# Kernel tuning notes

Hardware: AMD Instinct MI355X
Metric: run time of the kernel (lower is better)

## Reference

```python
import jax, jax.numpy as jnp
import numpy as np

N_NODES = 50000
N_GRAPHS = 100
NPG = 500          # nodes per graph
PAIRS = 2000       # undirected (src>dst) pairs per graph
E = N_GRAPHS * PAIRS * 2  # each pair duplicated with class 0/1 -> 400000 edges


def setup_inputs() -> dict:
    rng = np.random.default_rng(0)
    a = rng.integers(0, NPG, size=(N_GRAPHS, PAIRS))
    b = rng.integers(0, NPG - 1, size=(N_GRAPHS, PAIRS))
    b = b + (b >= a)                               # ensure b != a
    hi = np.maximum(a, b); lo = np.minimum(a, b)   # hi > lo  (src > dst)
    off = (np.arange(N_GRAPHS) * NPG)[:, None]
    hi = (hi + off).ravel(); lo = (lo + off).ravel()
    order = np.lexsort((lo, hi))                   # pre-sort by (row, col) -> sort_edge_index is identity
    hi, lo = hi[order], lo[order]
    src = np.repeat(hi, 2); dst = np.repeat(lo, 2)
    edges = np.stack([src, dst]).astype(np.int32)  # [2, E]
    weights = rng.random(E).astype(np.float32)
    classes = np.tile(np.array([0.0, 1.0], np.float32), E // 2)
    edge_attr = np.stack([weights, classes], axis=1)  # [E, 2]
    batch_labels = np.repeat(np.arange(N_GRAPHS), NPG).astype(np.int32)
    detector_labels = np.ones(N_NODES, dtype=bool)

    key = jax.random.key(0)
    ks = jax.random.split(key, 16)
    def lin(k, i, o):
        return jax.random.normal(k, (i, o), jnp.float32) * 0.1
    dims = [5, 32, 64, 128]
    p = {}
    for l in range(3):
        p[f"Wrel{l}"] = lin(ks[3 * l], dims[l], dims[l + 1])
        p[f"brel{l}"] = jnp.zeros((dims[l + 1],), jnp.float32)
        p[f"Wroot{l}"] = lin(ks[3 * l + 1], dims[l], dims[l + 1])
    p["Wd0"] = lin(ks[9], 257, 128); p["bd0"] = jnp.zeros((128,), jnp.float32)
    p["gnw0"] = jnp.ones((128,), jnp.float32); p["gnb0"] = jnp.zeros((128,), jnp.float32); p["gnms0"] = jnp.ones((128,), jnp.float32)
    p["Wd1"] = lin(ks[10], 128, 64); p["bd1"] = jnp.zeros((64,), jnp.float32)
    p["gnw1"] = jnp.ones((64,), jnp.float32); p["gnb1"] = jnp.zeros((64,), jnp.float32); p["gnms1"] = jnp.ones((64,), jnp.float32)
    p["Wout"] = lin(ks[11], 64, 1); p["bout"] = jnp.zeros((1,), jnp.float32)

    x = jax.random.normal(ks[12], (N_NODES, 5), jnp.float32)
    return dict(x=x, edges=jnp.asarray(edges), edge_attr=jnp.asarray(edge_attr),
                detector_labels=jnp.asarray(detector_labels),
                batch_labels=jnp.asarray(batch_labels), n_graphs=N_GRAPHS, **p)


def reference(x, edges, edge_attr, detector_labels, batch_labels, n_graphs,
              Wrel0, brel0, Wroot0, Wrel1, brel1, Wroot1, Wrel2, brel2, Wroot2,
              Wd0, bd0, gnw0, gnb0, gnms0, Wd1, bd1, gnw1, gnb1, gnms1, Wout, bout):
    N = x.shape[0]
    src, dst = edges[0], edges[1]
    w = edge_attr[:, :1]  # [E,1] edge weight

    # --- PyG GraphConv stack: out = segsum_dst(w * x[src]) @ W_rel + b_rel + x @ W_root ---
    for Wr, br, Wrt in ((Wrel0, brel0, Wroot0), (Wrel1, brel1, Wroot1), (Wrel2, brel2, Wroot2)):
        msg = x[src] * w                                   # gather + scale
        agg = jax.ops.segment_sum(msg, dst, num_segments=N)
        x = jnp.tanh(agg @ Wr + br + x @ Wrt)

    # --- SplitSyndromes: all nodes are detectors and all edges have src>dst by
    # construction, so the boolean compaction is the identity; sort_edge_index
    # is a stable sort by (row, col) ---
    order = jnp.lexsort((dst, src))
    src, dst = src[order], dst[order]
    ea = edge_attr[order]
    w = ea[:, :1]
    # (class_embd / weight_embd branches in the original are dead code: `c` is never used)

    feat = jnp.concatenate([x[src], w, x[dst]], axis=-1)   # [E, 257]
    eb = batch_labels[src]                                  # per-edge graph id

    def gnorm(h, wgt, bias, ms):
        # PyG GraphNorm: (h - mean*mean_scale) / sqrt(E[(h-mean*ms)^2] + 1e-5) * w + b, per graph
        cnt = jax.ops.segment_sum(jnp.ones(h.shape[0], h.dtype), eb, num_segments=n_graphs)
        mean = jax.ops.segment_sum(h, eb, num_segments=n_graphs) / cnt[:, None]
        out = h - mean[eb] * ms
        var = jax.ops.segment_sum(out * out, eb, num_segments=n_graphs) / cnt[:, None]
        return wgt * out / jnp.sqrt(var + 1e-5)[eb] + bias

    feat = gnorm(jnp.tanh(feat @ Wd0 + bd0), gnw0, gnb0, gnms0)
    feat = gnorm(jnp.tanh(feat @ Wd1 + bd1), gnw1, gnb1, gnms1)
    feat = feat @ Wout + bout                               # [E, 1]

    # --- pair consecutive (class 0/1) duplicates, take min, segment softmax ---
    pair = jnp.concatenate([feat[::2], feat[1::2]], axis=1)           # [E/2, 2]
    classes = jnp.stack([ea[::2, 1], ea[1::2, 1]], axis=1)           # [E/2, 2]
    vals = jnp.min(pair, axis=1)
    inds = jnp.argmin(pair, axis=1)
    edge_classes = jnp.take_along_axis(classes, inds[:, None], axis=1)[:, 0]
    out_edges = jnp.stack([src[::2], dst[::2]])
    ebp = batch_labels[src[::2]]
    m = jax.ops.segment_max(vals, ebp, num_segments=n_graphs)
    z = jnp.exp(vals - m[ebp])
    denom = jax.ops.segment_sum(z, ebp, num_segments=n_graphs)
    p = z / (denom[ebp] + 1e-16)                            # PyG softmax eps
    return out_edges, p, edge_classes
```

## Files before the change

### kernel.cpp

```cpp
#include <hip/hip_runtime.h>


#define N_NODES 50000
#define N_EDGES 400000
#define N_PAIRS 200000
#define N_G     100
#define EPG     4000
#define PPG     2000
#define NCHUNK  3125

typedef float  f4   __attribute__((ext_vector_type(4)));
typedef short  bf8  __attribute__((ext_vector_type(8)));
typedef unsigned u32x4 __attribute__((ext_vector_type(4)));
typedef unsigned short ushort_t;

__device__ __forceinline__ float tanh_fast(float x) {
    float cx = fminf(15.f, fmaxf(-15.f, x));
    float e = __expf(2.f * cx);
    return (e - 1.f) * __builtin_amdgcn_rcpf(e + 1.f);
}
__device__ __forceinline__ unsigned f2bf(float f) {
    unsigned u = __float_as_uint(f);
    return (u + 0x7FFFu + ((u >> 16) & 1u)) >> 16;
}
__device__ __forceinline__ float bf2f(unsigned h) { return __uint_as_float(h << 16); }

__global__ void k_csr_count(const int* __restrict__ edges, int* __restrict__ cnt) {
    int p = blockIdx.x * 256 + threadIdx.x;
    if (p >= N_PAIRS) return;
    atomicAdd(&cnt[edges[N_EDGES + 2 * p]], 1);
}
__global__ __launch_bounds__(512) void k_csr_scan(const int* __restrict__ cnt,
                                                  int* __restrict__ offs) {
    __shared__ int s[512];
    int g = blockIdx.x, t = threadIdx.x;
    int v = (t < 500) ? cnt[g * 500 + t] : 0;
    s[t] = v; __syncthreads();
    for (int off = 1; off < 512; off <<= 1) {
        int a = (t >= off) ? s[t - off] : 0;
        __syncthreads();
        s[t] += a; __syncthreads();
    }
    if (t < 500) offs[g * 500 + t] = g * PPG + s[t] - v;
}
__global__ void k_csr_fill(const int* __restrict__ edges, const float* __restrict__ ea,
                           const int* __restrict__ offs, int* __restrict__ fillc,
                           int* __restrict__ esrc, float* __restrict__ ew) {
    int p = blockIdx.x * 256 + threadIdx.x;
    if (p >= N_PAIRS) return;
    int d = edges[N_EDGES + 2 * p];
    int pos = offs[d] + atomicAdd(&fillc[d], 1);
    esrc[pos] = edges[2 * p];
    ew[pos] = ea[4 * p] + ea[4 * p + 2];
}

__global__ __launch_bounds__(256) void k_gath5(
    const int* __restrict__ cnt, const int* __restrict__ offs,
    const int* __restrict__ esrc, const float* __restrict__ ew,
    const float* __restrict__ x, float* __restrict__ agg) {
    int t = blockIdx.x * 256 + threadIdx.x;
    int n = t >> 3, k = t & 7;
    if (n >= N_NODES || k >= 5) return;
    int o0 = offs[n], c = cnt[n];
    float acc = 0.f;
    for (int i = o0; i < o0 + c; ++i) acc += x[esrc[i] * 5 + k] * ew[i];
    agg[n * 5 + k] = acc;
}
__global__ __launch_bounds__(256) void k_gath32(
    const int* __restrict__ cnt, const int* __restrict__ offs,
    const int* __restrict__ esrc, const float* __restrict__ ew,
    const float* __restrict__ x1, ushort_t* __restrict__ c2h, ushort_t* __restrict__ c2l) {
    int n = blockIdx.x * 8 + (threadIdx.x >> 5), k = threadIdx.x & 31;
    if (n >= N_NODES) return;
    int o0 = offs[n], c = cnt[n];
    float acc = 0.f;
    for (int i = o0; i < o0 + c; ++i) acc += x1[esrc[i] * 32 + k] * ew[i];
    unsigned hi = f2bf(acc);
    size_t o = (size_t)n * 64 + k;
    c2h[o] = (ushort_t)hi;
    c2l[o] = (ushort_t)f2bf(acc - bf2f(hi));
}
__global__ __launch_bounds__(256) void k_gath64(
    const int* __restrict__ cnt, const int* __restrict__ offs,
    const int* __restrict__ esrc, const float* __restrict__ ew,
    const float* __restrict__ x2, ushort_t* __restrict__ ch, ushort_t* __restrict__ cl) {
    int n = blockIdx.x * 4 + (threadIdx.x >> 6), k = threadIdx.x & 63;
    if (n >= N_NODES) return;
    int o0 = offs[n], c = cnt[n];
    float acc = 0.f;
    for (int i = o0; i < o0 + c; ++i) acc += x2[esrc[i] * 64 + k] * ew[i];
    unsigned hi = f2bf(acc);
    size_t o = (size_t)n * 128 + k;
    ch[o] = (ushort_t)hi;
    cl[o] = (ushort_t)f2bf(acc - bf2f(hi));
}

__global__ __launch_bounds__(256) void k_dense1(
    const float* __restrict__ x, const float* __restrict__ agg,
    const float* __restrict__ Wrel, const float* __restrict__ brel,
    const float* __restrict__ Wroot, float* __restrict__ x1,
    ushort_t* __restrict__ c2h, ushort_t* __restrict__ c2l) {
    __shared__ float wr[160], wt[160], bb[32];
    __shared__ float sa[8][5], sx[8][5];
    for (int i = threadIdx.x; i < 160; i += 256) { wr[i] = Wrel[i]; wt[i] = Wroot[i]; }
    if (threadIdx.x < 32) bb[threadIdx.x] = brel[threadIdx.x];
    int j = threadIdx.x & 31, nl = threadIdx.x >> 5;
    int nb = blockIdx.x * 8;
    __syncthreads();
    for (int i = threadIdx.x; i < 40; i += 256) {
        int nn = nb + i / 5, kk = i % 5;
        float av = 0.f, xv = 0.f;
        if (nn < N_NODES) { av = agg[nn * 5 + kk]; xv = x[nn * 5 + kk]; }
        sa[i / 5][kk] = av; sx[i / 5][kk] = xv;
    }
    __syncthreads();
    int n = nb + nl;
    if (n < N_NODES) {
        float acc = bb[j];
        #pragma unroll
        for (int k = 0; k < 5; ++k)
            acc += sa[nl][k] * wr[k * 32 + j] + sx[nl][k] * wt[k * 32 + j];
        float v = tanhf(acc);
        x1[n * 32 + j] = v;
        unsigned hi = f2bf(v);
        size_t o = (size_t)n * 64 + 32 + j;
        c2h[o] = (ushort_t)hi;
        c2l[o] = (ushort_t)f2bf(v - bf2f(hi));
    }
}

__global__ void k_packWc(const float* __restrict__ Wrel2, const float* __restrict__ Wroot2,
                         unsigned* __restrict__ dst) {
    int i = blockIdx.x * 256 + threadIdx.x;
    int t = i & 3, l = (i >> 2) & 63, kk = (i >> 8) & 3, n = i >> 10;
    int k = kk * 32 + ((l >> 4) << 3) + 2 * t;
    int j = 16 * n + (l & 15);
    float v0 = (k < 64) ? Wrel2[k * 128 + j] : Wroot2[(k - 64) * 128 + j];
    float v1 = (k + 1 < 64) ? Wrel2[(k + 1) * 128 + j] : Wroot2[(k + 1 - 64) * 128 + j];
    dst[i] = f2bf(v0) | (f2bf(v1) << 16);
}
__global__ void k_packWpq(const float* __restrict__ Wd0, unsigned* __restrict__ dst) {
    int i = blockIdx.x * 256 + threadIdx.x;
    int t = i & 3, l = (i >> 2) & 63, kk = (i >> 8) & 3, n = i >> 10;
    int k = kk * 32 + ((l >> 4) << 3) + 2 * t;
    int j = 16 * n + (l & 15);
    float v0 = (j < 128) ? Wd0[k * 128 + j] : Wd0[(129 + k) * 128 + (j - 128)];
    float v1 = (j < 128) ? Wd0[(k + 1) * 128 + j] : Wd0[(129 + k + 1) * 128 + (j - 128)];
    dst[i] = f2bf(v0) | (f2bf(v1) << 16);
}
__global__ void k_packW2(const float* __restrict__ Wrel1, const float* __restrict__ Wroot1,
                         unsigned* __restrict__ dst) {
    int i = blockIdx.x * 256 + threadIdx.x;
    int t = i & 3, l = (i >> 2) & 63, kk = (i >> 8) & 1, n = i >> 9;
    int k = kk * 32 + ((l >> 4) << 3) + 2 * t;
    int j = 16 * n + (l & 15);
    float v0 = (k < 32) ? Wrel1[k * 64 + j] : Wroot1[(k - 32) * 64 + j];
    float v1 = (k + 1 < 32) ? Wrel1[(k + 1) * 64 + j] : Wroot1[(k + 1 - 32) * 64 + j];
    dst[i] = f2bf(v0) | (f2bf(v1) << 16);
}

__global__ __launch_bounds__(256) void k_g1b(
    const ushort_t* __restrict__ Ah, const ushort_t* __restrict__ Al,
    const unsigned* __restrict__ Wb_, const float* __restrict__ bias,
    float* __restrict__ x2, ushort_t* __restrict__ ch, ushort_t* __restrict__ cl) {
    int wave = threadIdx.x >> 6, lane = threadIdx.x & 63;
    int rl = lane & 15, gp = lane >> 4;
    int cid = blockIdx.x * 4 + wave;
    if (cid >= NCHUNK) return;
    u32x4 B[4][2];
    const u32x4* Wb = (const u32x4*)Wb_;
    #pragma unroll
    for (int n = 0; n < 4; ++n)
        #pragma unroll
        for (int kk = 0; kk < 2; ++kk)
            B[n][kk] = Wb[(n * 2 + kk) * 64 + lane];
    float bs[4];
    #pragma unroll
    for (int n = 0; n < 4; ++n) bs[n] = bias[n * 16 + rl];
    const u32x4* ph = (const u32x4*)(Ah + (size_t)(cid * 16 + rl) * 64 + gp * 8);
    const u32x4* pl = (const u32x4*)(Al + (size_t)(cid * 16 + rl) * 64 + gp * 8);
    bf8 ah[2], al4[2];
    #pragma unroll
    for (int kk = 0; kk < 2; ++kk) {
        ah[kk]  = __builtin_bit_cast(bf8, ph[kk * 4]);
        al4[kk] = __builtin_bit_cast(bf8, pl[kk * 4]);
    }
    f4 acc[4];
    #pragma unroll
    for (int n = 0; n < 4; ++n) acc[n] = (f4)0.f;
    #pragma unroll
    for (int kk = 0; kk < 2; ++kk) {
        #pragma unroll
        for (int n = 0; n < 4; ++n)
            acc[n] = __builtin_amdgcn_mfma_f32_16x16x32_bf16(
                ah[kk], __builtin_bit_cast(bf8, B[n][kk]), acc[n], 0, 0, 0);
        #pragma unroll
        for (int n = 0; n < 4; ++n)
            acc[n] = __builtin_amdgcn_mfma_f32_16x16x32_bf16(
                al4[kk], __builtin_bit_cast(bf8, B[n][kk]), acc[n], 0, 0, 0);
    }
    #pragma unroll
    for (int n = 0; n < 4; ++n)
        #pragma unroll
        for (int t = 0; t < 4; ++t) {
            float v = tanh_fast(acc[n][t] + bs[n]);
            int node = cid * 16 + gp * 4 + t;
            int col = n * 16 + rl;
            x2[(size_t)node * 64 + col] = v;
            unsigned hi = f2bf(v);
            size_t o = (size_t)node * 128 + 64 + col;
            ch[o] = (ushort_t)hi;
            cl[o] = (ushort_t)f2bf(v - bf2f(hi));
        }
}

__global__ __launch_bounds__(256) void k_g1(
    const ushort_t* __restrict__ Ah, const ushort_t* __restrict__ Al,
    const unsigned* __restrict__ Wb_, const float* __restrict__ bias,
    ushort_t* __restrict__ Oh, ushort_t* __restrict__ Ol) {
    int wave = threadIdx.x >> 6, lane = threadIdx.x & 63;
    int cg = wave & 1, mg = wave >> 1;
    int rl = lane & 15, gp = lane >> 4;
    u32x4 B[4][4];
    const u32x4* Wb = (const u32x4*)Wb_;
    #pragma unroll
    for (int n = 0; n < 4; ++n)
        #pragma unroll
        for (int kk = 0; kk < 4; ++kk)
            B[n][kk] = Wb[((cg * 4 + n) * 4 + kk) * 64 + lane];
    float bs[4];
    #pragma unroll
    for (int n = 0; n < 4; ++n) bs[n] = bias[cg * 64 + n * 16 + rl];
    for (int it = 0; it < 2; ++it) {
        int cid = (blockIdx.x * 2 + it) * 2 + mg;
        if (cid >= NCHUNK) continue;
        const u32x4* ph = (const u32x4*)(Ah + (size_t)(cid * 16 + rl) * 128 + gp * 8);
        const u32x4* pl = (const u32x4*)(Al + (size_t)(cid * 16 + rl) * 128 + gp * 8);
        bf8 ah[4], al4[4];
        #pragma unroll
        for (int kk = 0; kk < 4; ++kk) {
            ah[kk]  = __builtin_bit_cast(bf8, ph[kk * 4]);
            al4[kk] = __builtin_bit_cast(bf8, pl[kk * 4]);
        }
        f4 acc[4];
        #pragma unroll
        for (int n = 0; n < 4; ++n) acc[n] = (f4)0.f;
        #pragma unroll
        for (int kk = 0; kk < 4; ++kk) {
            #pragma unroll
            for (int n = 0; n < 4; ++n)
                acc[n] = __builtin_amdgcn_mfma_f32_16x16x32_bf16(
                    ah[kk], __builtin_bit_cast(bf8, B[n][kk]), acc[n], 0, 0, 0);
            #pragma unroll
            for (int n = 0; n < 4; ++n)
                acc[n] = __builtin_amdgcn_mfma_f32_16x16x32_bf16(
                    al4[kk], __builtin_bit_cast(bf8, B[n][kk]), acc[n], 0, 0, 0);
        }
        #pragma unroll
        for (int n = 0; n < 4; ++n)
            #pragma unroll
            for (int t = 0; t < 4; ++t) {
                float v = tanh_fast(acc[n][t] + bs[n]);
                unsigned hi = f2bf(v);
                int node = cid * 16 + gp * 4 + t;
                int col = cg * 64 + n * 16 + rl;
                Oh[(size_t)node * 128 + col] = (ushort_t)hi;
                Ol[(size_t)node * 128 + col] = (ushort_t)f2bf(v - bf2f(hi));
            }
    }
}

__global__ __launch_bounds__(256) void k_g2(
    const ushort_t* __restrict__ Ah, const ushort_t* __restrict__ Al,
    const unsigned* __restrict__ Wb_, const float* __restrict__ bd0,
    float* __restrict__ P, float* __restrict__ Qb) {
    int cg = threadIdx.x >> 6, lane = threadIdx.x & 63;
    int rl = lane & 15, gp = lane >> 4;
    u32x4 B[4][4];
    const u32x4* Wb = (const u32x4*)Wb_;
    #pragma unroll
    for (int n = 0; n < 4; ++n)
        #pragma unroll
        for (int kk = 0; kk < 4; ++kk)
            B[n][kk] = Wb[((cg * 4 + n) * 4 + kk) * 64 + lane];
    float bs[4];
    #pragma unroll
    for (int n = 0; n < 4; ++n) {
        int j = cg * 64 + n * 16 + rl;
        bs[n] = (j < 128) ? bd0[j] : 0.f;
    }
    for (int it = 0; it < 2; ++it) {
        int cid = blockIdx.x * 2 + it;
        if (cid >= NCHUNK) continue;
        const u32x4* ph = (const u32x4*)(Ah + (size_t)(cid * 16 + rl) * 128 + gp * 8);
        const u32x4* pl = (const u32x4*)(Al + (size_t)(cid * 16 + rl) * 128 + gp * 8);
        bf8 ah[4], al4[4];
        #pragma unroll
        for (int kk = 0; kk < 4; ++kk) {
            ah[kk]  = __builtin_bit_cast(bf8, ph[kk * 4]);
            al4[kk] = __builtin_bit_cast(bf8, pl[kk * 4]);
        }
        f4 acc[4];
        #pragma unroll
        for (int n = 0; n < 4; ++n) acc[n] = (f4)0.f;
        #pragma unroll
        for (int kk = 0; kk < 4; ++kk) {
            #pragma unroll
            for (int n = 0; n < 4; ++n)
                acc[n] = __builtin_amdgcn_mfma_f32_16x16x32_bf16(
                    ah[kk], __builtin_bit_cast(bf8, B[n][kk]), acc[n], 0, 0, 0);
            #pragma unroll
            for (int n = 0; n < 4; ++n)
                acc[n] = __builtin_amdgcn_mfma_f32_16x16x32_bf16(
                    al4[kk], __builtin_bit_cast(bf8, B[n][kk]), acc[n], 0, 0, 0);
        }
        #pragma unroll
        for (int n = 0; n < 4; ++n) {
            int j = cg * 64 + n * 16 + rl;
            #pragma unroll
            for (int t = 0; t < 4; ++t) {
                float v = acc[n][t] + bs[n];
                int node = cid * 16 + gp * 4 + t;
                if (j < 128) P[(size_t)node * 128 + j] = v;
                else         Qb[(size_t)node * 128 + (j - 128)] = v;
            }
        }
    }
}

__global__ __launch_bounds__(256, 1) void k_h0s(
    const int* __restrict__ edges, const float* __restrict__ ea,
    const float* __restrict__ P, const float* __restrict__ Qb,
    const float* __restrict__ Wd0, float* __restrict__ part0) {
    __shared__ float ls[2][4][128];
    int g = blockIdx.x >> 3, tb = blockIdx.x & 7;
    int wave = threadIdx.x >> 6, lane = threadIdx.x & 63;
    int row = lane & 15, grp = lane >> 4;
    int slot = tb * 4 + wave;
    f4 wmr[4][2];
    #pragma unroll
    for (int kk = 0; kk < 4; ++kk) {
        const f4* wmp = (const f4*)(Wd0 + 16384 + kk * 32 + grp * 8);
        wmr[kk][0] = wmp[0]; wmr[kk][1] = wmp[1];
    }
    f4 s[4][2], q[4][2];
    #pragma unroll
    for (int kk = 0; kk < 4; ++kk)
        #pragma unroll
        for (int h = 0; h < 2; ++h) { s[kk][h] = (f4)0.f; q[kk][h] = (f4)0.f; }

    for (int j = 0; j < 4; ++j) {
        int tile = slot + 32 * j;
        if (tile >= 125) break;
        int eg0 = g * EPG + tile * 32;
        #pragma unroll
        for (int m = 0; m < 2; ++m) {
            int e = eg0 + 16 * m + row;
            int sn = edges[e], dn = edges[N_EDGES + e];
            float w = ea[2 * e];
            const f4* Pr = (const f4*)(P + sn * 128);
            const f4* Qr = (const f4*)(Qb + dn * 128);
            #pragma unroll
            for (int kk = 0; kk < 4; ++kk) {
                int o = kk * 8 + grp * 2;
                f4 p0 = Pr[o], p1 = Pr[o + 1];
                f4 q0 = Qr[o], q1 = Qr[o + 1];
                #pragma unroll
                for (int r = 0; r < 4; ++r) {
                    float h0 = tanh_fast(p0[r] + q0[r] + w * wmr[kk][0][r]);
                    float h1 = tanh_fast(p1[r] + q1[r] + w * wmr[kk][1][r]);
                    s[kk][0][r] += h0; q[kk][0][r] += h0 * h0;
                    s[kk][1][r] += h1; q[kk][1][r] += h1 * h1;
                }
            }
        }
    }
    #pragma unroll
    for (int kk = 0; kk < 4; ++kk)
        #pragma unroll
        for (int h = 0; h < 2; ++h)
            #pragma unroll
            for (int r = 0; r < 4; ++r) {
                float sv = s[kk][h][r], qv = q[kk][h][r];
                sv += __shfl_xor(sv, 1); sv += __shfl_xor(sv, 2);
                sv += __shfl_xor(sv, 4); sv += __shfl_xor(sv, 8);
                qv += __shfl_xor(qv, 1); qv += __shfl_xor(qv, 2);
                qv += __shfl_xor(qv, 4); qv += __shfl_xor(qv, 8);
                if (row == 0) {
                    int k = kk * 32 + grp * 8 + h * 4 + r;
                    ls[0][wave][k] = sv;
                    ls[1][wave][k] = qv;
                }
            }
    __syncthreads();
    int st = threadIdx.x >> 7, k = threadIdx.x & 127;
    float v = ls[st][0][k] + ls[st][1][k] + ls[st][2][k] + ls[st][3][k];
    part0[((size_t)(g * 8 + tb) * 2 + st) * 128 + k] = v;
}

__global__ __launch_bounds__(256) void k_fin0(
    const float* __restrict__ part0,
    const float* __restrict__ gnw, const float* __restrict__ gnb, const float* __restrict__ gnms,
    const float* __restrict__ Wd1, const float* __restrict__ bd1,
    unsigned* __restrict__ W1b, float* __restrict__ gam) {
    int g = blockIdx.x;
    __shared__ float al[128], be[128];
    if (threadIdx.x < 128) {
        int k = threadIdx.x;
        float S = 0.f, Q = 0.f;
        #pragma unroll
        for (int tb = 0; tb < 8; ++tb) {
            S += part0[((size_t)(g * 8 + tb) * 2 + 0) * 128 + k];
            Q += part0[((size_t)(g * 8 + tb) * 2 + 1) * 128 + k];
        }
        float mean = S * (1.f / EPG);
        float t = mean * gnms[k];
        float var = (Q - 2.f * t * S) * (1.f / EPG) + t * t;
        float a = gnw[k] * rsqrtf(var + 1e-5f);
        al[k] = a;
        be[k] = gnb[k] - a * t;
    }
    __syncthreads();
    unsigned* Wb = W1b + (size_t)g * 4096;
    for (int i = threadIdx.x; i < 4096; i += 256) {
        int t = i & 3, l = (i >> 2) & 63, kk = (i >> 8) & 3, n = i >> 10;
        int k = kk * 32 + ((l >> 4) << 3) + 2 * t;
        int j = 16 * n + (l & 15);
        unsigned lo = f2bf(al[k] * Wd1[k * 64 + j]);
        unsigned hi = f2bf(al[k + 1] * Wd1[(k + 1) * 64 + j]);
        Wb[i] = lo | (hi << 16);
    }
    if (threadIdx.x < 64) {
        int j = threadIdx.x;
        float acc = bd1[j];
        #pragma unroll 8
        for (int k = 0; k < 128; ++k) acc += be[k] * Wd1[k * 64 + j];
        gam[g * 64 + j] = acc;
    }
}

template<int DO_VALS, int STORE>
__global__ __launch_bounds__(256, 1) void k_h1m(
    const int* __restrict__ edges, const float* __restrict__ ea,
    const float* __restrict__ P, const float* __restrict__ Qb,
    const float* __restrict__ Wd0,
    const unsigned* __restrict__ W1b, const float* __restrict__ gam,
    const float* __restrict__ ug, const float* __restrict__ cg,
    float* __restrict__ part1,
    float* __restrict__ vals, float* __restrict__ outp, unsigned* __restrict__ h1ff) {
    __shared__ float ls[2][4][64];
    int g = blockIdx.x >> 3, tb = blockIdx.x & 7;
    int wave = threadIdx.x >> 6, lane = threadIdx.x & 63;
    int col = lane & 15, grp = lane >> 4;
    int slot = tb * 4 + wave;

    bf8 bfr[4][4];
    {
        const u32x4* Wb = (const u32x4*)(W1b + (size_t)g * 4096);
        #pragma unroll
        for (int n = 0; n < 4; ++n)
            #pragma unroll
            for (int kk = 0; kk < 4; ++kk)
                bfr[n][kk] = __builtin_bit_cast(bf8, Wb[(n * 4 + kk) * 64 + lane]);
    }
    f4 wmr[4][2];
    #pragma unroll
    for (int kk = 0; kk < 4; ++kk) {
        const f4* wmp = (const f4*)(Wd0 + 16384 + kk * 32 + grp * 8);
        wmr[kk][0] = wmp[0]; wmr[kk][1] = wmp[1];
    }
    float gamn[4], un[4] = {0.f, 0.f, 0.f, 0.f};
    #pragma unroll
    for (int n = 0; n < 4; ++n) gamn[n] = gam[g * 64 + 16 * n + col];
    float cgv = 0.f;
    if (DO_VALS) {
        #pragma unroll
        for (int n = 0; n < 4; ++n) un[n] = ug[g * 64 + 16 * n + col];
        cgv = cg[g];
    }
    float sacc[4] = {0.f, 0.f, 0.f, 0.f}, qacc[4] = {0.f, 0.f, 0.f, 0.f};

    for (int j = 0; j < 4; ++j) {
        int tile = slot + 32 * j;
        if (tile >= 125) break;
        int eg0 = g * EPG + tile * 32;
        bf8 af[2][4];
        #pragma unroll
        for (int m = 0; m < 2; ++m) {
            int e = eg0 + 16 * m + col;
            int sn = edges[e], dn = edges[N_EDGES + e];
            float w = ea[2 * e];
            const f4* Pr = (const f4*)(P + sn * 128);
            const f4* Qr = (const f4*)(Qb + dn * 128);
            #pragma unroll
            for (int kk = 0; kk < 4; ++kk) {
                int o = kk * 8 + grp * 2;
                f4 p0 = Pr[o], p1 = Pr[o + 1];
                f4 q0 = Qr[o], q1 = Qr[o + 1];
                bf8 a;
                #pragma unroll
                for (int r = 0; r < 4; ++r) {
                    float h0 = tanh_fast(p0[r] + q0[r] + w * wmr[kk][0][r]);
                    float h1 = tanh_fast(p1[r] + q1[r] + w * wmr[kk][1][r]);
                    a[r]     = (short)f2bf(h0);
                    a[4 + r] = (short)f2bf(h1);
                }
                af[m][kk] = a;
            }
        }
        f4 acc[2][4];
        #pragma unroll
        for (int m = 0; m < 2; ++m)
            #pragma unroll
            for (int n = 0; n < 4; ++n) acc[m][n] = (f4)0.f;
        #pragma unroll
        for (int kk = 0; kk < 4; ++kk)
            #pragma unroll
            for (int m = 0; m < 2; ++m)
                #pragma unroll
                for (int n = 0; n < 4; ++n)
                    acc[m][n] = __builtin_amdgcn_mfma_f32_16x16x32_bf16(
                        af[m][kk], bfr[n][kk], acc[m][n], 0, 0, 0);

        if (DO_VALS) {
            float rp[2][4];
            #pragma unroll
            for (int m = 0; m < 2; ++m)
                #pragma unroll
                for (int t = 0; t < 4; ++t) {
                    float v = 0.f;
                    #pragma unroll
                    for (int n = 0; n < 4; ++n)
                        v += un[n] * tanh_fast(acc[m][n][t] + gamn[n]);
                    v += __shfl_xor(v, 1); v += __shfl_xor(v, 2);
                    v += __shfl_xor(v, 4); v += __shfl_xor(v, 8);
                    rp[m][t] = v + cgv;
                }
            if (col == 0) {
                #pragma unroll
                for (int m = 0; m < 2; ++m)
                    #pragma unroll
                    for (int pr = 0; pr < 2; ++pr) {
                        float va = rp[m][2 * pr], vb = rp[m][2 * pr + 1];
                        int p = ((eg0 + 16 * m + grp * 4) >> 1) + pr;
                        vals[p] = fminf(va, vb);
                        outp[600000 + p] = (vb < va) ? 1.f : 0.f;
                        int e = 2 * p;
                        outp[p]          = (float)edges[e];
                        outp[200000 + p] = (float)edges[N_EDGES + e];
                    }
            }
        } else {
            int tileG = g * 125 + tile;
            #pragma unroll
            for (int m = 0; m < 2; ++m)
                #pragma unroll
                for (int n = 0; n < 4; ++n) {
                    float h[4];
                    #pragma unroll
                    for (int t = 0; t < 4; ++t) {
                        h[t] = tanh_fast(acc[m][n][t] + gamn[n]);
                        sacc[n] += h[t]; qacc[n] += h[t] * h[t];
                    }
                    if (STORE) {
                        unsigned w0 = f2bf(h[0]) | (f2bf(h[1]) << 16);
                        unsigned w1 = f2bf(h[2]) | (f2bf(h[3]) << 16);
                        size_t base = ((size_t)(tileG * 2 + m) * 4 + n) * 2;
                        h1ff[(base + 0) * 64 + lane] = w0;
                        h1ff[(base + 1) * 64 + lane] = w1;
                    }
                }
        }
    }
    if (!DO_VALS) {
        #pragma unroll
        for (int n = 0; n < 4; ++n) {
            float s = sacc[n], q = qacc[n];
            s += __shfl_xor(s, 16); s += __shfl_xor(s, 32);
            q += __shfl_xor(q, 16); q += __shfl_xor(q, 32);
            if (lane < 16) {
                ls[0][wave][n * 16 + col] = s;
                ls[1][wave][n * 16 + col] = q;
            }
        }
        __syncthreads();
        if (threadIdx.x < 128) {
            int st = threadIdx.x >> 6, k = threadIdx.x & 63;
            float v = ls[st][0][k] + ls[st][1][k] + ls[st][2][k] + ls[st][3][k];
            part1[((size_t)(g * 8 + tb) * 2 + st) * 64 + k] = v;
        }
    }
}

__global__ __launch_bounds__(256) void k_vals(
    const int* __restrict__ edges, const unsigned* __restrict__ h1ff,
    const float* __restrict__ ug, const float* __restrict__ cg,
    float* __restrict__ vals, float* __restrict__ outp) {
    int g = blockIdx.x >> 4, tb = blockIdx.x & 15;
    int wave = threadIdx.x >> 6, lane = threadIdx.x & 63;
    int col = lane & 15, grp = lane >> 4;
    int slot = tb * 4 + wave;
    float un[4];
    #pragma unroll
    for (int n = 0; n < 4; ++n) un[n] = ug[g * 64 + 16 * n + col];
    float cgv = cg[g];
    for (int j = 0; j < 2; ++j) {
        int tile = slot + 64 * j;
        if (tile >= 125) break;
        int tileG = g * 125 + tile;
        int eg0 = g * EPG + tile * 32;
        #pragma unroll
        for (int m = 0; m < 2; ++m) {
            float v[4] = {0.f, 0.f, 0.f, 0.f};
            #pragma unroll
            for (int n = 0; n < 4; ++n) {
                size_t base = ((size_t)(tileG * 2 + m) * 4 + n) * 2;
                unsigned w0 = h1ff[(base + 0) * 64 + lane];
                unsigned w1 = h1ff[(base + 1) * 64 + lane];
                v[0] += un[n] * bf2f(w0 & 0xFFFFu);
                v[1] += un[n] * bf2f(w0 >> 16);
                v[2] += un[n] * bf2f(w1 & 0xFFFFu);
                v[3] += un[n] * bf2f(w1 >> 16);
            }
            float rp[4];
            #pragma unroll
            for (int t = 0; t < 4; ++t) {
                float vv = v[t];
                vv += __shfl_xor(vv, 1); vv += __shfl_xor(vv, 2);
                vv += __shfl_xor(vv, 4); vv += __shfl_xor(vv, 8);
                rp[t] = vv + cgv;
            }
            if (col == 0) {
                #pragma unroll
                for (int pr = 0; pr < 2; ++pr) {
                    float va = rp[2 * pr], vb = rp[2 * pr + 1];
                    int p = ((eg0 + 16 * m + grp * 4) >> 1) + pr;
                    vals[p] = fminf(va, vb);
                    outp[600000 + p] = (vb < va) ? 1.f : 0.f;
                    int e = 2 * p;
                    outp[p]          = (float)edges[e];
                    outp[200000 + p] = (float)edges[N_EDGES + e];
                }
            }
        }
    }
}

__global__ void k_fin1(const float* __restrict__ part1,
                       const float* __restrict__ gnw, const float* __restrict__ gnb,
                       const float* __restrict__ gnms,
                       const float* __restrict__ Wout, const float* __restrict__ bout,
                       float* __restrict__ ug, float* __restrict__ cg) {
    int g = blockIdx.x; int j = threadIdx.x;
    float S = 0.f, Q = 0.f;
    #pragma unroll
    for (int tb = 0; tb < 8; ++tb) {
        S += part1[((size_t)(g * 8 + tb) * 2 + 0) * 64 + j];
        Q += part1[((size_t)(g * 8 + tb) * 2 + 1) * 64 + j];
    }
    float mean = S * (1.f / EPG);
    float t = mean * gnms[j];
    float var = (Q - 2.f * t * S) * (1.f / EPG) + t * t;
    float a = gnw[j] * rsqrtf(var + 1e-5f);
    float b = gnb[j] - a * t;
    ug[g * 64 + j] = a * Wout[j];
    float c = b * Wout[j];
    #pragma unroll
    for (int off = 32; off; off >>= 1) c += __shfl_xor(c, off);
    if (j == 0) cg[g] = c + bout[0];
}

__global__ __launch_bounds__(256) void k_softmax(const float* __restrict__ vals,
                                                 float* __restrict__ outp) {
    int g = blockIdx.x;
    __shared__ float rbuf[4], rbuf2[4];
    int t = threadIdx.x;
    const float* v = vals + g * PPG;
    float mx = -1e30f;
    for (int i = t; i < PPG; i += 256) mx = fmaxf(mx, v[i]);
    #pragma unroll
    for (int off = 32; off; off >>= 1) mx = fmaxf(mx, __shfl_xor(mx, off));
    if ((t & 63) == 0) rbuf[t >> 6] = mx;
    __syncthreads();
    mx = fmaxf(fmaxf(rbuf[0], rbuf[1]), fmaxf(rbuf[2], rbuf[3]));
    float sm = 0.f;
    for (int i = t; i < PPG; i += 256) sm += expf(v[i] - mx);
    #pragma unroll
    for (int off = 32; off; off >>= 1) sm += __shfl_xor(sm, off);
    if ((t & 63) == 0) rbuf2[t >> 6] = sm;
    __syncthreads();
    sm = rbuf2[0] + rbuf2[1] + rbuf2[2] + rbuf2[3];
    for (int i = t; i < PPG; i += 256)
        outp[400000 + g * PPG + i] = expf(v[i] - mx) / (sm + 1e-16f);
}

extern "C" void kernel_launch(void* const* d_in, const int* in_sizes, int n_in,
                              void* d_out, int out_size, void* d_ws, size_t ws_size,
                              hipStream_t stream) {
    const float* x     = (const float*)d_in[0];
    const int*   edges = (const int*)d_in[1];
    const float* ea    = (const float*)d_in[2];
    const float* Wrel0 = (const float*)d_in[6],  *brel0 = (const float*)d_in[7],  *Wroot0 = (const float*)d_in[8];
    const float* Wrel1 = (const float*)d_in[9],  *brel1 = (const float*)d_in[10], *Wroot1 = (const float*)d_in[11];
    const float* Wrel2 = (const float*)d_in[12], *brel2 = (const float*)d_in[13], *Wroot2 = (const float*)d_in[14];
    const float* Wd0 = (const float*)d_in[15],  *bd0 = (const float*)d_in[16];
    const float* gnw0 = (const float*)d_in[17], *gnb0 = (const float*)d_in[18], *gnms0 = (const float*)d_in[19];
    const float* Wd1 = (const float*)d_in[20],  *bd1 = (const float*)d_in[21];
    const float* gnw1 = (const float*)d_in[22], *gnb1 = (const float*)d_in[23], *gnms1 = (const float*)d_in[24];
    const float* Wout = (const float*)d_in[25], *bout = (const float*)d_in[26];
    float* o = (float*)d_out;
    float* w = (float*)d_ws;

    float* agg5 = w;
    float* x1   = w + 250000;
    float* x2   = w + 1850000;
    ushort_t* c2h = (ushort_t*)(w + 5050000);
    ushort_t* c2l = (ushort_t*)(w + 6650000);
    ushort_t* x3h = (ushort_t*)(w + 0);
    ushort_t* x3l = (ushort_t*)(w + 3200000);
    float* P    = w + 8250000;
    float* Qb   = w + 14650000;
    ushort_t* cath = (ushort_t*)(w + 8250000);
    ushort_t* catl = (ushort_t*)(w + 11450000);
    float* tail = w + 21050000;
    unsigned* Wcb  = (unsigned*)tail;
    unsigned* Wpqb = Wcb + 8192;
    unsigned* W2b  = Wpqb + 16384;
    int* cnt   = (int*)(W2b + 2048);
    int* fillc = cnt + 50000;
    int* offs  = fillc + 50000;
    int* esrc  = offs + 50000;
    float* ew  = (float*)(esrc + 200000);
    unsigned* W1b = (unsigned*)(ew + 200000);
    float* gam = (float*)(W1b + 409600);
    float* ug  = gam + 6400;
    float* cg  = ug + 6400;
    float* vals = cg + 100;
    float* part0 = vals + 200000;
    float* part1 = part0 + 204800;
    unsigned* h1ff = (unsigned*)(w + 25600000);
    const bool haveH1 = ws_size >= 155000000ULL;

    hipMemsetAsync(cnt, 0, 100000 * sizeof(int), stream);

    k_packWc<<<32, 256, 0, stream>>>(Wrel2, Wroot2, Wcb);
    k_packWpq<<<64, 256, 0, stream>>>(Wd0, Wpqb);
    k_packW2<<<8, 256, 0, stream>>>(Wrel1, Wroot1, W2b);

    k_csr_count<<<782, 256, 0, stream>>>(edges, cnt);
    k_csr_scan<<<N_G, 512, 0, stream>>>(cnt, offs);
    k_csr_fill<<<782, 256, 0, stream>>>(edges, ea, offs, fillc, esrc, ew);

    k_gath5<<<1563, 256, 0, stream>>>(cnt, offs, esrc, ew, x, agg5);
    k_dense1<<<6250, 256, 0, stream>>>(x, agg5, Wrel0, brel0, Wroot0, x1, c2h, c2l);
    k_gath32<<<6250, 256, 0, stream>>>(cnt, offs, esrc, ew, x1, c2h, c2l);
    k_g1b<<<782, 256, 0, stream>>>(c2h, c2l, W2b, brel1, x2, cath, catl);
    k_gath64<<<12500, 256, 0, stream>>>(cnt, offs, esrc, ew, x2, cath, catl);

    k_g1<<<(NCHUNK + 3) / 4, 256, 0, stream>>>(cath, catl, Wcb, brel2, x3h, x3l);
    k_g2<<<(NCHUNK + 1) / 2, 256, 0, stream>>>(x3h, x3l, Wpqb, bd0, P, Qb);

    k_h0s<<<N_G * 8, 256, 0, stream>>>(edges, ea, P, Qb, Wd0, part0);
    k_fin0<<<N_G, 256, 0, stream>>>(part0, gnw0, gnb0, gnms0, Wd1, bd1, W1b, gam);

    if (haveH1) {
        k_h1m<0, 1><<<N_G * 8, 256, 0, stream>>>(edges, ea, P, Qb, Wd0, W1b, gam,
                                                 ug, cg, part1, vals, o, h1ff);
        k_fin1<<<N_G, 64, 0, stream>>>(part1, gnw1, gnb1, gnms1, Wout, bout, ug, cg);
        k_vals<<<N_G * 16, 256, 0, stream>>>(edges, h1ff, ug, cg, vals, o);
    } else {
        k_h1m<0, 0><<<N_G * 8, 256, 0, stream>>>(edges, ea, P, Qb, Wd0, W1b, gam,
                                                 ug, cg, part1, vals, o, h1ff);
        k_fin1<<<N_G, 64, 0, stream>>>(part1, gnw1, gnb1, gnms1, Wout, bout, ug, cg);
        k_h1m<1, 0><<<N_G * 8, 256, 0, stream>>>(edges, ea, P, Qb, Wd0, W1b, gam,
                                                 ug, cg, part1, vals, o, h1ff);
    }

    k_softmax<<<N_G, 256, 0, stream>>>(vals, o);
}
```

Baseline: 394.8 us.

## Store P/Q node projections in bf16 and double per-graph block count

The node-level projections P and Q feeding the per-edge hidden-layer kernels are now written as bf16 instead of fp32. This halves the bytes of the random gathers in k_h0s and k_h1m, which unpack them back to fp32. Those kernels also launch 16 blocks per graph instead of 8, each covering fewer tiles, to raise parallelism. The partial-sum buffers and the reductions in fin0/fin1 are resized to match. The cost is reduced precision in the P+Q pre-activations.

```diff
diff --git a/kernel.cpp b/kernel.cpp
--- a/kernel.cpp
+++ b/kernel.cpp
@@ -24,6 +24,12 @@
     return (u + 0x7FFFu + ((u >> 16) & 1u)) >> 16;
 }
 __device__ __forceinline__ float bf2f(unsigned h) { return __uint_as_float(h << 16); }
+__device__ __forceinline__ void unp8(u32x4 v, f4& a, f4& b) {
+    a[0] = bf2f(v[0] & 0xFFFFu); a[1] = bf2f(v[0] >> 16);
+    a[2] = bf2f(v[1] & 0xFFFFu); a[3] = bf2f(v[1] >> 16);
+    b[0] = bf2f(v[2] & 0xFFFFu); b[1] = bf2f(v[2] >> 16);
+    b[2] = bf2f(v[3] & 0xFFFFu); b[3] = bf2f(v[3] >> 16);
+}
 
 __global__ void k_csr_count(const int* __restrict__ edges, int* __restrict__ cnt) {
     int p = blockIdx.x * 256 + threadIdx.x;
@@ -273,7 +279,7 @@
 __global__ __launch_bounds__(256) void k_g2(
     const ushort_t* __restrict__ Ah, const ushort_t* __restrict__ Al,
     const unsigned* __restrict__ Wb_, const float* __restrict__ bd0,
-    float* __restrict__ P, float* __restrict__ Qb) {
+    ushort_t* __restrict__ P16, ushort_t* __restrict__ Q16) {
     int cg = threadIdx.x >> 6, lane = threadIdx.x & 63;
     int rl = lane & 15, gp = lane >> 4;
     u32x4 B[4][4];
@@ -321,8 +327,8 @@
             for (int t = 0; t < 4; ++t) {
                 float v = acc[n][t] + bs[n];
                 int node = cid * 16 + gp * 4 + t;
-                if (j < 128) P[(size_t)node * 128 + j] = v;
-                else         Qb[(size_t)node * 128 + (j - 128)] = v;
+                if (j < 128) P16[(size_t)node * 128 + j] = (ushort_t)f2bf(v);
+                else         Q16[(size_t)node * 128 + (j - 128)] = (ushort_t)f2bf(v);
             }
         }
     }
@@ -330,10 +336,10 @@
 
 __global__ __launch_bounds__(256, 1) void k_h0s(
     const int* __restrict__ edges, const float* __restrict__ ea,
-    const float* __restrict__ P, const float* __restrict__ Qb,
+    const ushort_t* __restrict__ P16, const ushort_t* __restrict__ Q16,
     const float* __restrict__ Wd0, float* __restrict__ part0) {
     __shared__ float ls[2][4][128];
-    int g = blockIdx.x >> 3, tb = blockIdx.x & 7;
+    int g = blockIdx.x >> 4, tb = blockIdx.x & 15;
     int wave = threadIdx.x >> 6, lane = threadIdx.x & 63;
     int row = lane & 15, grp = lane >> 4;
     int slot = tb * 4 + wave;
@@ -349,8 +355,8 @@
         #pragma unroll
         for (int h = 0; h < 2; ++h) { s[kk][h] = (f4)0.f; q[kk][h] = (f4)0.f; }
 
-    for (int j = 0; j < 4; ++j) {
-        int tile = slot + 32 * j;
+    for (int j = 0; j < 2; ++j) {
+        int tile = slot + 64 * j;
         if (tile >= 125) break;
         int eg0 = g * EPG + tile * 32;
         #pragma unroll
@@ -358,13 +364,13 @@
             int e = eg0 + 16 * m + row;
             int sn = edges[e], dn = edges[N_EDGES + e];
             float w = ea[2 * e];
-            const f4* Pr = (const f4*)(P + sn * 128);
-            const f4* Qr = (const f4*)(Qb + dn * 128);
+            const u32x4* Pr = (const u32x4*)(P16 + (size_t)sn * 128);
+            const u32x4* Qr = (const u32x4*)(Q16 + (size_t)dn * 128);
             #pragma unroll
             for (int kk = 0; kk < 4; ++kk) {
-                int o = kk * 8 + grp * 2;
-                f4 p0 = Pr[o], p1 = Pr[o + 1];
-                f4 q0 = Qr[o], q1 = Qr[o + 1];
+                f4 p0, p1, q0, q1;
+                unp8(Pr[kk * 4 + grp], p0, p1);
+                unp8(Qr[kk * 4 + grp], q0, q1);
                 #pragma unroll
                 for (int r = 0; r < 4; ++r) {
                     float h0 = tanh_fast(p0[r] + q0[r] + w * wmr[kk][0][r]);
@@ -395,7 +401,7 @@
     __syncthreads();
     int st = threadIdx.x >> 7, k = threadIdx.x & 127;
     float v = ls[st][0][k] + ls[st][1][k] + ls[st][2][k] + ls[st][3][k];
-    part0[((size_t)(g * 8 + tb) * 2 + st) * 128 + k] = v;
+    part0[((size_t)(g * 16 + tb) * 2 + st) * 128 + k] = v;
 }
 
 __global__ __launch_bounds__(256) void k_fin0(
@@ -409,9 +415,9 @@
         int k = threadIdx.x;
         float S = 0.f, Q = 0.f;
         #pragma unroll
-        for (int tb = 0; tb < 8; ++tb) {
-            S += part0[((size_t)(g * 8 + tb) * 2 + 0) * 128 + k];
-            Q += part0[((size_t)(g * 8 + tb) * 2 + 1) * 128 + k];
+        for (int tb = 0; tb < 16; ++tb) {
+            S += part0[((size_t)(g * 16 + tb) * 2 + 0) * 128 + k];
+            Q += part0[((size_t)(g * 16 + tb) * 2 + 1) * 128 + k];
         }
         float mean = S * (1.f / EPG);
         float t = mean * gnms[k];
@@ -442,14 +448,14 @@
 template<int DO_VALS, int STORE>
 __global__ __launch_bounds__(256, 1) void k_h1m(
     const int* __restrict__ edges, const float* __restrict__ ea,
-    const float* __restrict__ P, const float* __restrict__ Qb,
+    const ushort_t* __restrict__ P16, const ushort_t* __restrict__ Q16,
     const float* __restrict__ Wd0,
     const unsigned* __restrict__ W1b, const float* __restrict__ gam,
     const float* __restrict__ ug, const float* __restrict__ cg,
     float* __restrict__ part1,
     float* __restrict__ vals, float* __restrict__ outp, unsigned* __restrict__ h1ff) {
     __shared__ float ls[2][4][64];
-    int g = blockIdx.x >> 3, tb = blockIdx.x & 7;
+    int g = blockIdx.x >> 4, tb = blockIdx.x & 15;
     int wave = threadIdx.x >> 6, lane = threadIdx.x & 63;
     int col = lane & 15, grp = lane >> 4;
     int slot = tb * 4 + wave;
@@ -480,8 +486,8 @@
     }
     float sacc[4] = {0.f, 0.f, 0.f, 0.f}, qacc[4] = {0.f, 0.f, 0.f, 0.f};
 
-    for (int j = 0; j < 4; ++j) {
-        int tile = slot + 32 * j;
+    for (int j = 0; j < 2; ++j) {
+        int tile = slot + 64 * j;
         if (tile >= 125) break;
         int eg0 = g * EPG + tile * 32;
         bf8 af[2][4];
@@ -490,13 +496,13 @@
             int e = eg0 + 16 * m + col;
             int sn = edges[e], dn = edges[N_EDGES + e];
             float w = ea[2 * e];
-            const f4* Pr = (const f4*)(P + sn * 128);
-            const f4* Qr = (const f4*)(Qb + dn * 128);
+            const u32x4* Pr = (const u32x4*)(P16 + (size_t)sn * 128);
+            const u32x4* Qr = (const u32x4*)(Q16 + (size_t)dn * 128);
             #pragma unroll
             for (int kk = 0; kk < 4; ++kk) {
-                int o = kk * 8 + grp * 2;
-                f4 p0 = Pr[o], p1 = Pr[o + 1];
-                f4 q0 = Qr[o], q1 = Qr[o + 1];
+                f4 p0, p1, q0, q1;
+                unp8(Pr[kk * 4 + grp], p0, p1);
+                unp8(Qr[kk * 4 + grp], q0, q1);
                 bf8 a;
                 #pragma unroll
                 for (int r = 0; r < 4; ++r) {
@@ -587,7 +593,7 @@
         if (threadIdx.x < 128) {
             int st = threadIdx.x >> 6, k = threadIdx.x & 63;
             float v = ls[st][0][k] + ls[st][1][k] + ls[st][2][k] + ls[st][3][k];
-            part1[((size_t)(g * 8 + tb) * 2 + st) * 64 + k] = v;
+            part1[((size_t)(g * 16 + tb) * 2 + st) * 64 + k] = v;
         }
     }
 }
@@ -654,9 +660,9 @@
     int g = blockIdx.x; int j = threadIdx.x;
     float S = 0.f, Q = 0.f;
     #pragma unroll
-    for (int tb = 0; tb < 8; ++tb) {
-        S += part1[((size_t)(g * 8 + tb) * 2 + 0) * 64 + j];
-        Q += part1[((size_t)(g * 8 + tb) * 2 + 1) * 64 + j];
+    for (int tb = 0; tb < 16; ++tb) {
+        S += part1[((size_t)(g * 16 + tb) * 2 + 0) * 64 + j];
+        Q += part1[((size_t)(g * 16 + tb) * 2 + 1) * 64 + j];
     }
     float mean = S * (1.f / EPG);
     float t = mean * gnms[j];
@@ -718,10 +724,10 @@
     ushort_t* c2l = (ushort_t*)(w + 6650000);
     ushort_t* x3h = (ushort_t*)(w + 0);
     ushort_t* x3l = (ushort_t*)(w + 3200000);
-    float* P    = w + 8250000;
-    float* Qb   = w + 14650000;
     ushort_t* cath = (ushort_t*)(w + 8250000);
     ushort_t* catl = (ushort_t*)(w + 11450000);
+    ushort_t* P16  = (ushort_t*)(w + 8250000);
+    ushort_t* Q16  = (ushort_t*)(w + 11450000);
     float* tail = w + 21050000;
     unsigned* Wcb  = (unsigned*)tail;
     unsigned* Wpqb = Wcb + 8192;
@@ -737,7 +743,7 @@
     float* cg  = ug + 6400;
     float* vals = cg + 100;
     float* part0 = vals + 200000;
-    float* part1 = part0 + 204800;
+    float* part1 = part0 + 409600;
     unsigned* h1ff = (unsigned*)(w + 25600000);
     const bool haveH1 = ws_size >= 155000000ULL;
 
@@ -758,22 +764,22 @@
     k_gath64<<<12500, 256, 0, stream>>>(cnt, offs, esrc, ew, x2, cath, catl);
 
     k_g1<<<(NCHUNK + 3) / 4, 256, 0, stream>>>(cath, catl, Wcb, brel2, x3h, x3l);
-    k_g2<<<(NCHUNK + 1) / 2, 256, 0, stream>>>(x3h, x3l, Wpqb, bd0, P, Qb);
-
-    k_h0s<<<N_G * 8, 256, 0, stream>>>(edges, ea, P, Qb, Wd0, part0);
+    k_g2<<<(NCHUNK + 1) / 2, 256, 0, stream>>>(x3h, x3l, Wpqb, bd0, P16, Q16);
+
+    k_h0s<<<N_G * 16, 256, 0, stream>>>(edges, ea, P16, Q16, Wd0, part0);
     k_fin0<<<N_G, 256, 0, stream>>>(part0, gnw0, gnb0, gnms0, Wd1, bd1, W1b, gam);
 
     if (haveH1) {
-        k_h1m<0, 1><<<N_G * 8, 256, 0, stream>>>(edges, ea, P, Qb, Wd0, W1b, gam,
-                                                 ug, cg, part1, vals, o, h1ff);
+        k_h1m<0, 1><<<N_G * 16, 256, 0, stream>>>(edges, ea, P16, Q16, Wd0, W1b, gam,
+                                                  ug, cg, part1, vals, o, h1ff);
         k_fin1<<<N_G, 64, 0, stream>>>(part1, gnw1, gnb1, gnms1, Wout, bout, ug, cg);
         k_vals<<<N_G * 16, 256, 0, stream>>>(edges, h1ff, ug, cg, vals, o);
     } else {
-        k_h1m<0, 0><<<N_G * 8, 256, 0, stream>>>(edges, ea, P, Qb, Wd0, W1b, gam,
-                                                 ug, cg, part1, vals, o, h1ff);
+        k_h1m<0, 0><<<N_G * 16, 256, 0, stream>>>(edges, ea, P16, Q16, Wd0, W1b, gam,
+                                                  ug, cg, part1, vals, o, h1ff);
         k_fin1<<<N_G, 64, 0, stream>>>(part1, gnw1, gnb1, gnms1, Wout, bout, ug, cg);
-        k_h1m<1, 0><<<N_G * 8, 256, 0, stream>>>(edges, ea, P, Qb, Wd0, W1b, gam,
-                                                 ug, cg, part1, vals, o, h1ff);
+        k_h1m<1, 0><<<N_G * 16, 256, 0, stream>>>(edges, ea, P16, Q16, Wd0, W1b, gam,
+                                                  ug, cg, part1, vals, o, h1ff);
     }
 
     k_softmax<<<N_G, 256, 0, stream>>>(vals, o);
```

Result: faster. 376.2 us (-4.7%).
